# Optimization experiments

Measured on AMD Instinct MI355X. Metric: run time of the kernel, lower is better.

## Reference

```python
import jax, jax.numpy as jnp
import numpy as np

K = 4  # number of processing steps (init kwarg)


def setup_inputs() -> dict:
    key = jax.random.key(0)
    ks = jax.random.split(key, 6)
    B, S, D = 4096, 8192, 512
    H = D  # hidden_size == input_size (residual h + f_x)
    scale = 1.0 / np.sqrt(H)
    return {
        "f_x": jax.random.normal(ks[0], (B, D), dtype=jnp.float32),
        "g_S": jax.random.normal(ks[1], (S, D), dtype=jnp.float32),
        # LSTM step: input f_x (size D), 'hidden' is concat([h, r]) of size 2H
        "W_ih": jax.random.uniform(ks[2], (4 * H, D), jnp.float32, -scale, scale),
        "W_hh": jax.random.uniform(ks[3], (4 * H, 2 * H), jnp.float32, -scale, scale),
        "b_ih": jax.random.uniform(ks[4], (4 * H,), jnp.float32, -scale, scale),
        "b_hh": jax.random.uniform(ks[5], (4 * H,), jnp.float32, -scale, scale),
    }


def _lstm_step(x, hidden, c, W_ih, W_hh, b_ih, b_hh):
    # gates: [B, 4H]; PyTorch LSTMCell gate order (i, f, g, o)
    gates = x @ W_ih.T + b_ih + hidden @ W_hh.T + b_hh
    i, f, g, o = jnp.split(gates, 4, axis=1)
    c_new = jax.nn.sigmoid(f) * c + jax.nn.sigmoid(i) * jnp.tanh(g)
    h_new = jax.nn.sigmoid(o) * jnp.tanh(c_new)
    return h_new, c_new


def reference(f_x, g_S, W_ih, W_hh, b_ih, b_hh):
    # f_x: [B, D] queries; g_S: [S, D] support set embeddings
    h = f_x
    c = jnp.zeros_like(f_x)
    for _ in range(K):
        a = jax.nn.softmax(h @ g_S.T, axis=1)       # [B, S] attention over support
        r = a @ g_S                                  # [B, D] attention readout
        concat = jnp.concatenate([h, r], axis=1)     # [B, 2D]
        h, c = _lstm_step(f_x, concat, c, W_ih, W_hh, b_ih, b_hh)
        h = h + f_x                                  # residual skip connection
    return h
```

## Files before the change

kernel.cpp:

```cpp
#include <hip/hip_runtime.h>

typedef _Float16 f16x8 __attribute__((ext_vector_type(8)));
typedef _Float16 f16x4 __attribute__((ext_vector_type(4)));
typedef float f32x4 __attribute__((ext_vector_type(4)));

#define S_DIM 8192
#define D_DIM 512

__device__ __forceinline__ void gload_lds16(const _Float16* g, _Float16* l) {
  __builtin_amdgcn_global_load_lds(
      (const __attribute__((address_space(1))) unsigned int*)g,
      (__attribute__((address_space(3))) unsigned int*)l, 16, 0, 0);
}

__device__ __forceinline__ float sigf(float x) { return 1.0f / (1.0f + __expf(-x)); }
__device__ __forceinline__ float tanhfast(float x) {
  return 1.0f - 2.0f / (__expf(2.0f * x) + 1.0f);
}


template <int BM, int BN>
__global__ __launch_bounds__(256) void gemm_bt(const _Float16* __restrict__ A, int lda,
                                               const _Float16* __restrict__ B, int ldb,
                                               _Float16* __restrict__ C, int ldc, int K) {
  constexpr int BK = 64;
  constexpr int FM = BM / 32, FN = BN / 32;
  __shared__ _Float16 As[BM * BK];
  __shared__ _Float16 Bs[BN * BK];
  const int tid = threadIdx.x;
  const int lane = tid & 63;
  const int wv = tid >> 6;
  const int bm = blockIdx.y * BM;
  const int bn = blockIdx.x * BN;
  const int wm = (wv >> 1) * (BM / 2);
  const int wn = (wv & 1) * (BN / 2);
  const int fr = lane & 15;
  const int hi4 = lane >> 4;
  const int rx7 = fr & 7;
  const int srow = lane >> 3;
  const int schk = (lane & 7) ^ srow;

  f32x4 acc[FM][FN] = {};

  for (int kt = 0; kt < K; kt += BK) {
    __syncthreads();
#pragma unroll
    for (int p = 0; p < BM / 32; ++p) {
      const int m = wv + 4 * p;
      gload_lds16(A + (size_t)(bm + 8 * m + srow) * lda + kt + schk * 8, As + 512 * m);
    }
#pragma unroll
    for (int p = 0; p < BN / 32; ++p) {
      const int m = wv + 4 * p;
      gload_lds16(B + (size_t)(bn + 8 * m + srow) * ldb + kt + schk * 8, Bs + 512 * m);
    }
    __syncthreads();

#pragma unroll
    for (int h = 0; h < 2; ++h) {
      const int co = (((h << 2) | hi4) ^ rx7) << 3;
      f16x8 af[FM], bf[FN];
#pragma unroll
      for (int i = 0; i < FM; ++i)
        af[i] = *(const f16x8*)&As[(wm + i * 16 + fr) * 64 + co];
#pragma unroll
      for (int j = 0; j < FN; ++j)
        bf[j] = *(const f16x8*)&Bs[(wn + j * 16 + fr) * 64 + co];
#pragma unroll
      for (int i = 0; i < FM; ++i)
#pragma unroll
        for (int j = 0; j < FN; ++j)
          acc[i][j] = __builtin_amdgcn_mfma_f32_16x16x32_f16(af[i], bf[j], acc[i][j], 0, 0, 0);
    }
  }

  const int cc = lane & 15;
  const int cr = (lane >> 4) * 4;
#pragma unroll
  for (int i = 0; i < FM; ++i)
#pragma unroll
    for (int j = 0; j < FN; ++j) {
      size_t base = (size_t)(bm + wm + i * 16 + cr) * ldc + (bn + wn + j * 16 + cc);
#pragma unroll
      for (int r = 0; r < 4; ++r) C[base + (size_t)r * ldc] = (_Float16)acc[i][j][r];
    }
}

__global__ __launch_bounds__(256) void gemm_rsplit(const _Float16* __restrict__ A,
                                                   const _Float16* __restrict__ B,
                                                   float* __restrict__ Ppart) {
  constexpr int BK = 64;
  __shared__ _Float16 As[128 * BK];
  __shared__ _Float16 Bs[64 * BK];
  const int tid = threadIdx.x;
  const int lane = tid & 63;
  const int wv = tid >> 6;
  const int bm = blockIdx.x * 128;
  const int bn = blockIdx.y * 64;
  const int kc = blockIdx.z;
  const int k0 = kc * 1024;
  const int wm = (wv >> 1) * 64;
  const int wn = (wv & 1) * 32;
  const int fr = lane & 15;
  const int hi4 = lane >> 4;
  const int rx7 = fr & 7;
  const int srow = lane >> 3;
  const int schk = (lane & 7) ^ srow;

  f32x4 acc[4][2] = {};

  for (int kt = k0; kt < k0 + 1024; kt += BK) {
    __syncthreads();
#pragma unroll
    for (int p = 0; p < 4; ++p) {
      const int m = wv + 4 * p;
      gload_lds16(A + (size_t)(bm + 8 * m + srow) * 16384 + kt + schk * 8, As + 512 * m);
    }
#pragma unroll
    for (int p = 0; p < 2; ++p) {
      const int m = wv + 4 * p;
      gload_lds16(B + (size_t)(bn + 8 * m + srow) * 8192 + kt + schk * 8, Bs + 512 * m);
    }
    __syncthreads();

#pragma unroll
    for (int h = 0; h < 2; ++h) {
      const int co = (((h << 2) | hi4) ^ rx7) << 3;
      f16x8 af[4], bf[2];
#pragma unroll
      for (int i = 0; i < 4; ++i)
        af[i] = *(const f16x8*)&As[(wm + i * 16 + fr) * 64 + co];
#pragma unroll
      for (int j = 0; j < 2; ++j)
        bf[j] = *(const f16x8*)&Bs[(wn + j * 16 + fr) * 64 + co];
#pragma unroll
      for (int i = 0; i < 4; ++i)
#pragma unroll
        for (int j = 0; j < 2; ++j)
          acc[i][j] = __builtin_amdgcn_mfma_f32_16x16x32_f16(af[i], bf[j], acc[i][j], 0, 0, 0);
    }
  }

  const int cc = lane & 15;
  const int cr = (lane >> 4) * 4;
#pragma unroll
  for (int i = 0; i < 4; ++i)
#pragma unroll
    for (int j = 0; j < 2; ++j) {
      size_t base = (size_t)(bm + wm + i * 16 + cr) * 8192 + 4096 + (size_t)kc * 512 +
                    (bn + wn + j * 16 + cc);
#pragma unroll
      for (int r = 0; r < 4; ++r) Ppart[base + (size_t)r * 8192] = acc[i][j][r];
    }
}

__global__ __launch_bounds__(256) void reduce_r(const float* __restrict__ Ppart,
                                                _Float16* __restrict__ rout) {
  int idx = blockIdx.x * 256 + threadIdx.x;
  int m = idx >> 7;
  int n4 = (idx & 127) * 4;
  const float* base = Ppart + (size_t)m * 8192 + 4096 + n4;
  f32x4 s = {0.f, 0.f, 0.f, 0.f};
#pragma unroll
  for (int kc = 0; kc < 8; ++kc) s += *(const f32x4*)(base + kc * 512);
  f16x4 h = {(_Float16)s[0], (_Float16)s[1], (_Float16)s[2], (_Float16)s[3]};
  *(f16x4*)&rout[(size_t)m * 1024 + n4] = h;
}

__global__ __launch_bounds__(512) void gemm_scores2(const _Float16* __restrict__ Ah,
                                                    const _Float16* __restrict__ Al,
                                                    const _Float16* __restrict__ Bh,
                                                    float* __restrict__ C) {
  __shared__ _Float16 As[2][256 * 64];
  __shared__ _Float16 Bs[2][256 * 64];
  const int tid = threadIdx.x;
  const int lane = tid & 63;
  const int wv = tid >> 6;
  const int bm = blockIdx.y * 256;
  const int bn = blockIdx.x * 256;
  const int wm = (wv >> 2) * 128;
  const int wn = (wv & 3) * 64;
  const int fr = lane & 15;
  const int hi4 = lane >> 4;
  const int rx7 = fr & 7;
  const int srow = lane >> 3;
  const int schk = (lane & 7) ^ srow;

  f32x4 acc[8][4] = {};

  auto stage_q = [&](int t, int q, _Float16* nA, _Float16* nB) {
    const int m = wv + 8 * q;
    const int k0 = t * 64;
    const _Float16* asrc =
        (t < 8) ? Ah + (size_t)(bm + 8 * m + srow) * 1024 + k0 + schk * 8
                : Al + (size_t)(bm + 8 * m + srow) * 512 + (k0 - 512) + schk * 8;
    gload_lds16(asrc, nA + 512 * m);
    gload_lds16(Bh + (size_t)(bn + 8 * m + srow) * 512 + (t & 7) * 64 + schk * 8,
                nB + 512 * m);
  };

  auto tile = [&](int t, const _Float16* cA, const _Float16* cB, _Float16* nA,
                  _Float16* nB) {
#pragma unroll
    for (int q = 0; q < 4; ++q) {
      if (t < 15) stage_q(t + 1, q, nA, nB);
      f16x8 af[2][2], bf[4][2];
#pragma unroll
      for (int ii = 0; ii < 2; ++ii)
#pragma unroll
        for (int h = 0; h < 2; ++h)
          af[ii][h] = *(const f16x8*)&cA[(wm + (2 * q + ii) * 16 + fr) * 64 +
                                         ((((h << 2) | hi4) ^ rx7) << 3)];
#pragma unroll
      for (int j = 0; j < 4; ++j)
#pragma unroll
        for (int h = 0; h < 2; ++h)
          bf[j][h] = *(const f16x8*)&cB[(wn + j * 16 + fr) * 64 +
                                        ((((h << 2) | hi4) ^ rx7) << 3)];
      __builtin_amdgcn_s_setprio(1);
#pragma unroll
      for (int ii = 0; ii < 2; ++ii)
#pragma unroll
        for (int j = 0; j < 4; ++j) {
          acc[2 * q + ii][j] = __builtin_amdgcn_mfma_f32_16x16x32_f16(
              af[ii][0], bf[j][0], acc[2 * q + ii][j], 0, 0, 0);
          acc[2 * q + ii][j] = __builtin_amdgcn_mfma_f32_16x16x32_f16(
              af[ii][1], bf[j][1], acc[2 * q + ii][j], 0, 0, 0);
        }
      __builtin_amdgcn_s_setprio(0);
    }
    __syncthreads();
  };

#pragma unroll
  for (int q = 0; q < 4; ++q) stage_q(0, q, As[0], Bs[0]);
  __syncthreads();

  for (int tt = 0; tt < 16; tt += 2) {
    tile(tt, As[0], Bs[0], As[1], Bs[1]);
    tile(tt + 1, As[1], Bs[1], As[0], Bs[0]);
  }

  const int cc = lane & 15;
  const int cr = (lane >> 4) * 4;
#pragma unroll
  for (int i = 0; i < 8; ++i)
#pragma unroll
    for (int j = 0; j < 4; ++j) {
      size_t base = (size_t)(bm + wm + i * 16 + cr) * 8192 + (bn + wn + j * 16 + cc);
#pragma unroll
      for (int r = 0; r < 4; ++r) C[base + (size_t)r * 8192] = acc[i][j][r];
    }
}

__global__ __launch_bounds__(256) void prep_g(const float* __restrict__ g,
                                              _Float16* __restrict__ gT,
                                              _Float16* __restrict__ g_h) {
  __shared__ _Float16 tile[64][72];
  const int s0 = blockIdx.x * 64;
  const int d0 = blockIdx.y * 64;
  const int t = threadIdx.x;
  const int r = t >> 2;
  const int cq = (t & 3) * 16;
  alignas(16) _Float16 buf[16];
#pragma unroll
  for (int q = 0; q < 4; ++q) {
    f32x4 v = *(const f32x4*)&g[(size_t)(s0 + r) * D_DIM + d0 + cq + q * 4];
#pragma unroll
    for (int e = 0; e < 4; ++e) buf[q * 4 + e] = (_Float16)v[e];
  }
#pragma unroll
  for (int k = 0; k < 16; ++k) tile[r][cq + k] = buf[k];
  *(f16x8*)&g_h[(size_t)(s0 + r) * D_DIM + d0 + cq] = *(const f16x8*)&buf[0];
  *(f16x8*)&g_h[(size_t)(s0 + r) * D_DIM + d0 + cq + 8] = *(const f16x8*)&buf[8];
  __syncthreads();
  alignas(16) _Float16 ob[16];
#pragma unroll
  for (int k = 0; k < 16; ++k) ob[k] = tile[cq + k][r];
  *(f16x8*)&gT[(size_t)(d0 + r) * S_DIM + s0 + cq] = *(const f16x8*)&ob[0];
  *(f16x8*)&gT[(size_t)(d0 + r) * S_DIM + s0 + cq + 8] = *(const f16x8*)&ob[8];
}

__global__ __launch_bounds__(256) void prep_misc(const float* __restrict__ W_ih,
                                                 const float* __restrict__ W_hh,
                                                 const float* __restrict__ f_x,
                                                 _Float16* __restrict__ wih_h,
                                                 _Float16* __restrict__ whh_h,
                                                 _Float16* __restrict__ concat,
                                                 _Float16* __restrict__ h_lo,
                                                 float* __restrict__ c) {
  const int NW1 = 2048 * 512 / 4;
  const int NW2 = 2048 * 1024 / 4;
  const int NFX = 4096 * 512 / 4;
  int idx = blockIdx.x * 256 + threadIdx.x;
  if (idx < NW1) {
    f32x4 v = ((const f32x4*)W_ih)[idx];
    f16x4 h = {(_Float16)v[0], (_Float16)v[1], (_Float16)v[2], (_Float16)v[3]};
    ((f16x4*)wih_h)[idx] = h;
  } else if (idx < NW1 + NW2) {
    int k = idx - NW1;
    f32x4 v = ((const f32x4*)W_hh)[k];
    f16x4 h = {(_Float16)v[0], (_Float16)v[1], (_Float16)v[2], (_Float16)v[3]};
    ((f16x4*)whh_h)[k] = h;
  } else if (idx < NW1 + NW2 + NFX) {
    int k = idx - NW1 - NW2;
    f32x4 v = ((const f32x4*)f_x)[k];
    f16x4 h, lo;
#pragma unroll
    for (int e = 0; e < 4; ++e) {
      h[e] = (_Float16)v[e];
      lo[e] = (_Float16)(v[e] - (float)h[e]);
    }
    int m = k >> 7, j4 = k & 127;
    ((f16x4*)concat)[m * 256 + j4] = h;
    ((f16x4*)h_lo)[k] = lo;
    f32x4 z = {0.f, 0.f, 0.f, 0.f};
    ((f32x4*)c)[k] = z;
  }
}

__global__ __launch_bounds__(256) void softmax_inplace(float* __restrict__ P) {
  float* p = P + (size_t)blockIdx.x * S_DIM;
  const int tid = threadIdx.x, lane = tid & 63, wave = tid >> 6;
  __shared__ float red[8];
  float x[32];
#pragma unroll
  for (int i = 0; i < 8; ++i) {
    f32x4 v = *(const f32x4*)&p[i * 1024 + tid * 4];
#pragma unroll
    for (int j = 0; j < 4; ++j) x[i * 4 + j] = v[j];
  }
  float m = -3.0e38f;
#pragma unroll
  for (int k = 0; k < 32; ++k) m = fmaxf(m, x[k]);
#pragma unroll
  for (int o = 32; o; o >>= 1) m = fmaxf(m, __shfl_xor(m, o));
  if (lane == 0) red[wave] = m;
  __syncthreads();
  m = fmaxf(fmaxf(red[0], red[1]), fmaxf(red[2], red[3]));
  float s = 0.f;
#pragma unroll
  for (int k = 0; k < 32; ++k) {
    x[k] = exp2f((x[k] - m) * 1.44269504f);
    s += x[k];
  }
#pragma unroll
  for (int o = 32; o; o >>= 1) s += __shfl_xor(s, o);
  if (lane == 0) red[4 + wave] = s;
  __syncthreads();
  s = (red[4] + red[5]) + (red[6] + red[7]);
  float inv = 1.0f / s;
  _Float16* out = (_Float16*)p;
#pragma unroll
  for (int i = 0; i < 8; ++i) {
    f16x4 v;
#pragma unroll
    for (int j = 0; j < 4; ++j) v[j] = (_Float16)(x[i * 4 + j] * inv);
    *(f16x4*)&out[i * 1024 + tid * 4] = v;
  }
}

__global__ __launch_bounds__(256) void lstm_step(const _Float16* __restrict__ gmm,
                                                 const _Float16* __restrict__ gbase,
                                                 const float* __restrict__ b_ih,
                                                 const float* __restrict__ b_hh,
                                                 const float* __restrict__ f_x,
                                                 float* __restrict__ c,
                                                 _Float16* __restrict__ concat,
                                                 _Float16* __restrict__ h_lo,
                                                 float* __restrict__ hout) {
  int idx = blockIdx.x * 256 + threadIdx.x;
  int m = idx >> 7;
  int j = (idx & 127) * 4;
  size_t grow = (size_t)m * 2048 + j;
  f16x4 gI = *(const f16x4*)&gmm[grow];
  f16x4 gF = *(const f16x4*)&gmm[grow + 512];
  f16x4 gG = *(const f16x4*)&gmm[grow + 1024];
  f16x4 gO = *(const f16x4*)&gmm[grow + 1536];
  f16x4 aI = *(const f16x4*)&gbase[grow];
  f16x4 aF = *(const f16x4*)&gbase[grow + 512];
  f16x4 aG = *(const f16x4*)&gbase[grow + 1024];
  f16x4 aO = *(const f16x4*)&gbase[grow + 1536];
  f32x4 biI = *(const f32x4*)&b_ih[j];
  f32x4 biF = *(const f32x4*)&b_ih[j + 512];
  f32x4 biG = *(const f32x4*)&b_ih[j + 1024];
  f32x4 biO = *(const f32x4*)&b_ih[j + 1536];
  f32x4 bhI = *(const f32x4*)&b_hh[j];
  f32x4 bhF = *(const f32x4*)&b_hh[j + 512];
  f32x4 bhG = *(const f32x4*)&b_hh[j + 1024];
  f32x4 bhO = *(const f32x4*)&b_hh[j + 1536];
  f32x4 cv = ((const f32x4*)c)[idx];
  f32x4 fx = ((const f32x4*)f_x)[idx];
  f32x4 cn, hn;
  f16x4 h16, l16;
#pragma unroll
  for (int k = 0; k < 4; ++k) {
    float gi = (float)gI[k] + (float)aI[k] + biI[k] + bhI[k];
    float gf = (float)gF[k] + (float)aF[k] + biF[k] + bhF[k];
    float gg = (float)gG[k] + (float)aG[k] + biG[k] + bhG[k];
    float go = (float)gO[k] + (float)aO[k] + biO[k] + bhO[k];
    float ci = sigf(gf) * cv[k] + sigf(gi) * tanhfast(gg);
    float hi = sigf(go) * tanhfast(ci) + fx[k];
    cn[k] = ci;
    hn[k] = hi;
    h16[k] = (_Float16)hi;
    l16[k] = (_Float16)(hi - (float)h16[k]);
  }
  ((f32x4*)c)[idx] = cn;
  ((f32x4*)hout)[idx] = hn;
  ((f16x4*)concat)[m * 256 + (idx & 127)] = h16;
  ((f16x4*)h_lo)[idx] = l16;
}

extern "C" void kernel_launch(void* const* d_in, const int* in_sizes, int n_in,
                              void* d_out, int out_size, void* d_ws, size_t ws_size,
                              hipStream_t stream) {
  const float* f_x = (const float*)d_in[0];
  const float* g_S = (const float*)d_in[1];
  const float* W_ih = (const float*)d_in[2];
  const float* W_hh = (const float*)d_in[3];
  const float* b_ih = (const float*)d_in[4];
  const float* b_hh = (const float*)d_in[5];
  float* hout = (float*)d_out;

  char* w = (char*)d_ws;
  float* P32 = (float*)w;
  _Float16* gates = (_Float16*)w;
  _Float16* gbase = (_Float16*)(w + 67108864);
  _Float16* concat = (_Float16*)(w + 83886080);
  _Float16* g_h = (_Float16*)(w + 92274688);
  _Float16* gT = (_Float16*)(w + 109051904);
  _Float16* wih_h = (_Float16*)(w + 117440512);
  _Float16* whh_h = (_Float16*)(w + 119537664);
  float* c = (float*)(w + 123731968);
  _Float16* h_lo = (_Float16*)(w + 132120576);

  prep_g<<<dim3(S_DIM / 64, D_DIM / 64), 256, 0, stream>>>(g_S, gT, g_h);
  prep_misc<<<5120, 256, 0, stream>>>(W_ih, W_hh, f_x, wih_h, whh_h, concat, h_lo, c);

  gemm_bt<128, 128><<<dim3(2048 / 128, 4096 / 128), 256, 0, stream>>>(
      concat, 1024, wih_h, 512, gbase, 2048, 512);

  for (int it = 0; it < 4; ++it) {
    for (int hb = 0; hb < 2; ++hb) {
      const _Float16* hhi = concat + (size_t)hb * 2048 * 1024;
      const _Float16* hlo = h_lo + (size_t)hb * 2048 * 512;
      gemm_scores2<<<dim3(32, 8), 512, 0, stream>>>(hhi, hlo, g_h, P32);
      softmax_inplace<<<2048, 256, 0, stream>>>(P32);
      gemm_rsplit<<<dim3(16, 8, 8), 256, 0, stream>>>((const _Float16*)P32, gT, P32);
      reduce_r<<<1024, 256, 0, stream>>>(P32, concat + (size_t)hb * 2048 * 1024 + 512);
    }
    gemm_bt<128, 128><<<dim3(2048 / 128, 4096 / 128), 256, 0, stream>>>(
        concat, 1024, whh_h, 1024, gates, 2048, 1024);
    lstm_step<<<2048, 256, 0, stream>>>(gates, gbase, b_ih, b_hh, f_x, c, concat, h_lo, hout);
  }
  (void)in_sizes; (void)n_in; (void)out_size; (void)ws_size;
}
```

Baseline: 887.0 us.

## Restructure scores GEMM pipeline with two-tiles-ahead prefetch and explicit vmcnt waits

The scores GEMM now issues global-to-LDS loads for tile t+2 into the buffer just consumed, instead of interleaving t+1 loads with compute. It uses raw s_barrier plus explicit s_waitcnt vmcnt(8) so the next tile's loads can stay in flight across the barrier. B fragments are also hoisted out of the q loop so they are read from LDS once per tile rather than four times. This aims to hide global load latency and cut LDS read traffic. The cost is a reliance on manual wait counts that must exactly match the number of outstanding loads.

```diff
diff --git a/kernel.cpp b/kernel.cpp
--- a/kernel.cpp
+++ b/kernel.cpp
@@ -167,7 +167,7 @@
   *(f16x4*)&rout[(size_t)m * 1024 + n4] = h;
 }
 
-__global__ __launch_bounds__(512) void gemm_scores2(const _Float16* __restrict__ Ah,
+__global__ __launch_bounds__(512) void gemm_scores3(const _Float16* __restrict__ Ah,
                                                     const _Float16* __restrict__ Al,
                                                     const _Float16* __restrict__ Bh,
                                                     float* __restrict__ C) {
@@ -188,35 +188,37 @@
 
   f32x4 acc[8][4] = {};
 
-  auto stage_q = [&](int t, int q, _Float16* nA, _Float16* nB) {
-    const int m = wv + 8 * q;
+  auto stage = [&](int t, _Float16* dA, _Float16* dB) {
     const int k0 = t * 64;
-    const _Float16* asrc =
-        (t < 8) ? Ah + (size_t)(bm + 8 * m + srow) * 1024 + k0 + schk * 8
-                : Al + (size_t)(bm + 8 * m + srow) * 512 + (k0 - 512) + schk * 8;
-    gload_lds16(asrc, nA + 512 * m);
-    gload_lds16(Bh + (size_t)(bn + 8 * m + srow) * 512 + (t & 7) * 64 + schk * 8,
-                nB + 512 * m);
+#pragma unroll
+    for (int q = 0; q < 4; ++q) {
+      const int m = wv + 8 * q;
+      const _Float16* asrc =
+          (t < 8) ? Ah + (size_t)(bm + 8 * m + srow) * 1024 + k0 + schk * 8
+                  : Al + (size_t)(bm + 8 * m + srow) * 512 + (k0 - 512) + schk * 8;
+      gload_lds16(asrc, dA + 512 * m);
+      gload_lds16(Bh + (size_t)(bn + 8 * m + srow) * 512 + (t & 7) * 64 + schk * 8,
+                  dB + 512 * m);
+    }
   };
 
-  auto tile = [&](int t, const _Float16* cA, const _Float16* cB, _Float16* nA,
-                  _Float16* nB) {
+  auto compute = [&](const _Float16* cA, const _Float16* cB) {
+    f16x8 bf[4][2];
+#pragma unroll
+    for (int j = 0; j < 4; ++j)
+#pragma unroll
+      for (int h = 0; h < 2; ++h)
+        bf[j][h] = *(const f16x8*)&cB[(wn + j * 16 + fr) * 64 +
+                                      ((((h << 2) | hi4) ^ rx7) << 3)];
 #pragma unroll
     for (int q = 0; q < 4; ++q) {
-      if (t < 15) stage_q(t + 1, q, nA, nB);
-      f16x8 af[2][2], bf[4][2];
+      f16x8 af[2][2];
 #pragma unroll
       for (int ii = 0; ii < 2; ++ii)
 #pragma unroll
         for (int h = 0; h < 2; ++h)
           af[ii][h] = *(const f16x8*)&cA[(wm + (2 * q + ii) * 16 + fr) * 64 +
                                          ((((h << 2) | hi4) ^ rx7) << 3)];
-#pragma unroll
-      for (int j = 0; j < 4; ++j)
-#pragma unroll
-        for (int h = 0; h < 2; ++h)
-          bf[j][h] = *(const f16x8*)&cB[(wn + j * 16 + fr) * 64 +
-                                        ((((h << 2) | hi4) ^ rx7) << 3)];
       __builtin_amdgcn_s_setprio(1);
 #pragma unroll
       for (int ii = 0; ii < 2; ++ii)
@@ -229,16 +231,31 @@
         }
       __builtin_amdgcn_s_setprio(0);
     }
-    __syncthreads();
   };
 
-#pragma unroll
-  for (int q = 0; q < 4; ++q) stage_q(0, q, As[0], Bs[0]);
-  __syncthreads();
+  auto step = [&](int t, _Float16* bA, _Float16* bB) {
+    compute(bA, bB);
+    __builtin_amdgcn_s_barrier();
+    if (t + 2 < 16) stage(t + 2, bA, bB);
+    __builtin_amdgcn_sched_barrier(0);
+    if (t + 2 < 16)
+      asm volatile("s_waitcnt vmcnt(8)" ::: "memory");
+    else
+      asm volatile("s_waitcnt vmcnt(0)" ::: "memory");
+    __builtin_amdgcn_s_barrier();
+    __builtin_amdgcn_sched_barrier(0);
+  };
+
+  stage(0, As[0], Bs[0]);
+  stage(1, As[1], Bs[1]);
+  __builtin_amdgcn_sched_barrier(0);
+  asm volatile("s_waitcnt vmcnt(8)" ::: "memory");
+  __builtin_amdgcn_s_barrier();
+  __builtin_amdgcn_sched_barrier(0);
 
   for (int tt = 0; tt < 16; tt += 2) {
-    tile(tt, As[0], Bs[0], As[1], Bs[1]);
-    tile(tt + 1, As[1], Bs[1], As[0], Bs[0]);
+    step(tt, As[0], Bs[0]);
+    step(tt + 1, As[1], Bs[1]);
   }
 
   const int cc = lane & 15;
@@ -445,7 +462,7 @@
     for (int hb = 0; hb < 2; ++hb) {
       const _Float16* hhi = concat + (size_t)hb * 2048 * 1024;
       const _Float16* hlo = h_lo + (size_t)hb * 2048 * 512;
-      gemm_scores2<<<dim3(32, 8), 512, 0, stream>>>(hhi, hlo, g_h, P32);
+      gemm_scores3<<<dim3(32, 8), 512, 0, stream>>>(hhi, hlo, g_h, P32);
       softmax_inplace<<<2048, 256, 0, stream>>>(P32);
       gemm_rsplit<<<dim3(16, 8, 8), 256, 0, stream>>>((const _Float16*)P32, gT, P32);
       reduce_r<<<1024, 256, 0, stream>>>(P32, concat + (size_t)hb * 2048 * 1024 + 512);
```

Measured after the change: 875.1 us. No clear change (-1.3%).
